# Optimization experiments

Hardware: AMD Instinct MI355X
Metric: run time of the kernel (lower is better)

The kernel has to match this reference:

```python
import jax, jax.numpy as jnp
import numpy as np

B, S, D, H = 4, 2048, 1024, 16
HD = D // H


def setup_inputs() -> dict:
    key = jax.random.key(0)
    ks = jax.random.split(key, 6)
    scale = 1.0 / np.sqrt(D)
    return {
        'x': jax.random.normal(ks[0], (B, S, D), dtype=jnp.float32),
        'wq': jax.random.normal(ks[1], (D, D), dtype=jnp.float32) * scale,
        'wk': jax.random.normal(ks[2], (D, D), dtype=jnp.float32) * scale,
        'wv': jax.random.normal(ks[3], (D, D), dtype=jnp.float32) * scale,
        'wo': jax.random.normal(ks[4], (D, D), dtype=jnp.float32) * scale,
        'wo_b': jnp.zeros((D,), dtype=jnp.float32),
    }


def reference(x, wq, wk, wv, wo, wo_b):
    b, s, _ = x.shape
    # Linear projections (torch Linear: x @ W.T), reshape to [b, h, s, hd]
    def proj(w):
        return jnp.einsum('bsd,ed->bse', x, w).reshape(b, s, H, HD).transpose(0, 2, 1, 3)
    q, k, v = proj(wq), proj(wk), proj(wv)
    scores = jnp.einsum('bhqd,bhkd->bhqk', q, k)  # [b,h,s,s]
    causal = jnp.triu(jnp.ones((s, s), dtype=bool), k=1)
    scores = jnp.where(causal, -jnp.inf, scores)
    attn = jax.nn.softmax(scores / np.sqrt(HD), axis=-1)
    ctx = jnp.einsum('bhqk,bhkd->bhqd', attn, v)  # [b,h,s,hd]
    ctx = ctx.transpose(0, 2, 1, 3).reshape(b, s, D)
    return jnp.einsum('bsd,ed->bse', ctx, wo) + wo_b
```

## Files before the change

kernel.cpp:

```cpp
#include <hip/hip_runtime.h>

#define SB 4
#define SS 2048
#define SD 1024
#define SH 16
#define SHD 64
#define SM (SB * SS)

typedef __bf16 bf16x8 __attribute__((ext_vector_type(8)));
typedef float f32x4 __attribute__((ext_vector_type(4)));

static __device__ __forceinline__ unsigned short f2bf(float x) {
    unsigned int u = __builtin_bit_cast(unsigned int, x);
    u += 0x7fffu + ((u >> 16) & 1u);
    return (unsigned short)(u >> 16);
}

static __device__ __forceinline__ float fast_exp2(float x) {
#if __has_builtin(__builtin_amdgcn_exp2f)
    return __builtin_amdgcn_exp2f(x);
#else
    return exp2f(x);
#endif
}

static __device__ __forceinline__ unsigned int pkhi(float a, float b) {
    return __builtin_amdgcn_perm(__builtin_bit_cast(unsigned int, a),
                                 __builtin_bit_cast(unsigned int, b), 0x07060302u);
}

typedef __attribute__((address_space(1))) void GV;
typedef __attribute__((address_space(3))) void LV;

static __device__ __forceinline__ void async16(const void* g, void* l) {
    __builtin_amdgcn_global_load_lds((GV*)g, (LV*)l, 16, 0, 0);
}

#define QSCALE 0.18033688011112042f

__global__ __launch_bounds__(256) void cast_all(
    const float* __restrict__ x,  const float* __restrict__ wq,
    const float* __restrict__ wk, const float* __restrict__ wv,
    const float* __restrict__ wo,
    unsigned short* __restrict__ xb, unsigned short* __restrict__ wqkv,
    unsigned short* __restrict__ wo16) {
    int i = blockIdx.x * 256 + threadIdx.x;
    const float4* src;
    ushort4* dst;
    if (i < 2097152) {
        src = reinterpret_cast<const float4*>(x) + i;
        dst = reinterpret_cast<ushort4*>(xb) + i;
    } else {
        int j = i - 2097152;
        int which = j >> 18;
        int r = j & 262143;
        const float* ws_[4] = {wq, wk, wv, wo};
        src = reinterpret_cast<const float4*>(ws_[which]) + r;
        dst = (which < 3 ? reinterpret_cast<ushort4*>(wqkv) + which * 262144
                         : reinterpret_cast<ushort4*>(wo16)) + r;
    }
    float4 v = *src;
    ushort4 o;
    o.x = f2bf(v.x); o.y = f2bf(v.y); o.z = f2bf(v.z); o.w = f2bf(v.w);
    *dst = o;
}

#define NT16 (SD / 64)

__device__ __forceinline__ void gemm_mainloop(
    const unsigned short* __restrict__ A,
    const unsigned short* __restrict__ Bt,
    int tileM, int tileN, int tid,
    unsigned short* As0, unsigned short* As1, unsigned short* As2,
    unsigned short* Bs0, unsigned short* Bs1,
    f32x4 (&acc)[4][4]) {

    const int lane = tid & 63;
    const int quad = lane >> 4;
    const int col0 = lane & 15;
    const int w = tid >> 6;
    const int wm = w >> 1;
    const int wn = w & 1;

    const int r0 = tid >> 3;
    const int cc = ((tid & 7) ^ (r0 & 7)) * 8;

    const unsigned short* gA0 = A + (size_t)(tileM + r0) * SD + cc;
    const unsigned short* gA1 = gA0 + (size_t)64 * SD;
    const unsigned short* gA2 = gA0 + (size_t)128 * SD;
    const unsigned short* gA3 = gA0 + (size_t)192 * SD;
    const unsigned short* gB0 = Bt + (size_t)(tileN + r0) * SD + cc;
    const unsigned short* gB1 = gB0 + (size_t)64 * SD;

    unsigned short* const Asb[3] = {As0, As1, As2};
    unsigned short* const Bsb[2] = {Bs0, Bs1};
    const int t16 = tid * 16;

    const int cs0 = (quad ^ (col0 & 7)) * 16;
    const int cs1 = ((4 + quad) ^ (col0 & 7)) * 16;
    const int arow = (wm * 64 + col0) * 128;
    const int brow = (wn * 64 + col0) * 128;

#define STAGE_A(t, Asx) do {                                         \
        async16(gA0 + (t) * 64, (char*)(Asx) + t16);                 \
        async16(gA1 + (t) * 64, (char*)(Asx) + 8192 + t16);          \
        async16(gA2 + (t) * 64, (char*)(Asx) + 16384 + t16);         \
        async16(gA3 + (t) * 64, (char*)(Asx) + 24576 + t16);         \
    } while (0)
#define STAGE_B(t, Bsx) do {                                         \
        async16(gB0 + (t) * 64, (char*)(Bsx) + t16);                 \
        async16(gB1 + (t) * 64, (char*)(Bsx) + 8192 + t16);          \
    } while (0)

    STAGE_A(0, As0);
    STAGE_B(0, Bs0);
    STAGE_A(1, As1);

#pragma unroll
    for (int t = 0; t < NT16; ++t) {
        if (t + 1 < NT16)
            asm volatile("s_waitcnt vmcnt(4)" ::: "memory");
        else
            asm volatile("s_waitcnt vmcnt(0)" ::: "memory");
        __builtin_amdgcn_s_barrier();
        __builtin_amdgcn_sched_barrier(0);

        const unsigned short* As = Asb[t % 3];
        const unsigned short* Bs = Bsb[t & 1];

        bf16x8 af[4][2], bfr[4][2];
#pragma unroll
        for (int fr = 0; fr < 4; ++fr) {
            const char* rp = (const char*)As + arow + fr * 2048;
            af[fr][0] = *reinterpret_cast<const bf16x8*>(rp + cs0);
            af[fr][1] = *reinterpret_cast<const bf16x8*>(rp + cs1);
        }
#pragma unroll
        for (int fc = 0; fc < 4; ++fc) {
            const char* rp = (const char*)Bs + brow + fc * 2048;
            bfr[fc][0] = *reinterpret_cast<const bf16x8*>(rp + cs0);
            bfr[fc][1] = *reinterpret_cast<const bf16x8*>(rp + cs1);
        }

        if (t + 1 < NT16) STAGE_B(t + 1, Bsb[(t + 1) & 1]);
        if (t + 2 < NT16) STAGE_A(t + 2, Asb[(t + 2) % 3]);

        __builtin_amdgcn_s_setprio(1);
#pragma unroll
        for (int ks = 0; ks < 2; ++ks)
#pragma unroll
            for (int fr = 0; fr < 4; ++fr)
#pragma unroll
                for (int fc = 0; fc < 4; ++fc)
                    acc[fr][fc] = __builtin_amdgcn_mfma_f32_16x16x32_bf16(
                        af[fr][ks], bfr[fc][ks], acc[fr][fc], 0, 0, 0);
        __builtin_amdgcn_s_setprio(0);
    }
#undef STAGE_A
#undef STAGE_B
}

__global__ __launch_bounds__(512, 2) void gemm_qkv(
    const unsigned short* __restrict__ xb,
    const unsigned short* __restrict__ wqkv,
    unsigned short* __restrict__ Qd,
    unsigned short* __restrict__ Kd,
    unsigned short* __restrict__ Vtd) {

    __shared__ __align__(16) unsigned short As0[256 * 64];
    __shared__ __align__(16) unsigned short As1[256 * 64];
    __shared__ __align__(16) unsigned short As2[256 * 64];
    __shared__ __align__(16) unsigned short Bs0[128 * 64];
    __shared__ __align__(16) unsigned short Bs1[128 * 64];
    const int tid = threadIdx.x;
    const int tileN = blockIdx.x * 128;
    const int tileM = blockIdx.y * 256;

    f32x4 acc[4][4];
    const f32x4 z = {0.f, 0.f, 0.f, 0.f};
#pragma unroll
    for (int i = 0; i < 4; ++i)
#pragma unroll
        for (int j = 0; j < 4; ++j) acc[i][j] = z;

    gemm_mainloop(xb, wqkv, tileM, tileN, tid, As0, As1, As2, Bs0, Bs1, acc);

    const int lane = tid & 63, quad = lane >> 4, col0 = lane & 15;
    const int w = tid >> 6, wm = w >> 1, wn = w & 1;

#pragma unroll
    for (int ct = 0; ct < 4; ++ct) {
        int n0 = tileN + wn * 64 + ct * 16;
        int which = n0 >> 10;
        int e0 = n0 & 1023;
        int h = e0 >> 6;
        int hd = (e0 & 63) + col0;
#pragma unroll
        for (int rt = 0; rt < 4; ++rt) {
            int m0 = tileM + wm * 64 + rt * 16 + quad * 4;
            int bb = m0 >> 11;
            int s0 = m0 & 2047;
            int bh = bb * SH + h;
            if (which == 0) {
                int base = (bh * SS + s0) * SHD + hd;
#pragma unroll
                for (int r = 0; r < 4; ++r)
                    Qd[base + r * SHD] = f2bf(acc[rt][ct][r] * QSCALE);
            } else if (which == 1) {
                int base = (bh * SS + s0) * SHD + hd;
#pragma unroll
                for (int r = 0; r < 4; ++r)
                    Kd[base + r * SHD] = f2bf(acc[rt][ct][r]);
            } else {
                int base = (bh * SHD + hd) * SS + s0;
                ushort4 pk;
                pk.x = f2bf(acc[rt][ct][0]);
                pk.y = f2bf(acc[rt][ct][1]);
                pk.z = f2bf(acc[rt][ct][2]);
                pk.w = f2bf(acc[rt][ct][3]);
                *reinterpret_cast<ushort4*>(Vtd + base) = pk;
            }
        }
    }
}

__global__ __launch_bounds__(512, 2) void gemm_out(
    const unsigned short* __restrict__ ctx,
    const unsigned short* __restrict__ wo16,
    const float* __restrict__ wb,
    float* __restrict__ out) {

    __shared__ __align__(16) unsigned short As0[256 * 64];
    __shared__ __align__(16) unsigned short As1[256 * 64];
    __shared__ __align__(16) unsigned short As2[256 * 64];
    __shared__ __align__(16) unsigned short Bs0[128 * 64];
    __shared__ __align__(16) unsigned short Bs1[128 * 64];
    const int tid = threadIdx.x;
    const int tileN = blockIdx.x * 128;
    const int tileM = blockIdx.y * 256;

    f32x4 acc[4][4];
    const f32x4 z = {0.f, 0.f, 0.f, 0.f};
#pragma unroll
    for (int i = 0; i < 4; ++i)
#pragma unroll
        for (int j = 0; j < 4; ++j) acc[i][j] = z;

    gemm_mainloop(ctx, wo16, tileM, tileN, tid, As0, As1, As2, Bs0, Bs1, acc);

    const int lane = tid & 63, quad = lane >> 4, col0 = lane & 15;
    const int w = tid >> 6, wm = w >> 1, wn = w & 1;

#pragma unroll
    for (int ct = 0; ct < 4; ++ct) {
        int n = tileN + wn * 64 + ct * 16 + col0;
        float bias = wb[n];
#pragma unroll
        for (int rt = 0; rt < 4; ++rt) {
            int m0 = tileM + wm * 64 + rt * 16 + quad * 4;
#pragma unroll
            for (int r = 0; r < 4; ++r)
                out[(size_t)(m0 + r) * SD + n] = acc[rt][ct][r] + bias;
        }
    }
}

#define PSTR 72

__device__ __forceinline__ void stage_kv(
    const unsigned short* __restrict__ Kg,
    const unsigned short* __restrict__ Vtg,
    size_t base, int t, int srow0, int scs, int tid,
    unsigned short* Kb, unsigned short* Vb) {
#pragma unroll
    for (int j = 0; j < 2; ++j) {
        int row = j * 32 + srow0;
        int chunk = scs ^ (row & 7);
        int slot16 = (j * 256 + tid) * 16;
        async16(Kg + base + (size_t)(t * 64 + row) * SHD + chunk * 8,
                (char*)Kb + slot16);
        async16(Vtg + base + (size_t)row * SS + t * 64 + chunk * 8,
                (char*)Vb + slot16);
    }
}

__device__ __forceinline__ void attn_tile(
    const unsigned short* __restrict__ Kc,
    const unsigned short* __restrict__ Vc,
    int kb, int q0, int quad, int col0,
    const bf16x8 (&bq)[2][2], const bf16x8& ones,
    unsigned short* Psw, f32x4 (&ot)[2][4], f32x4 (&lacc)[2]) {

    const f32x4 z = {0.f, 0.f, 0.f, 0.f};

    bf16x8 ak[4][2];
#pragma unroll
    for (int rt = 0; rt < 4; ++rt)
#pragma unroll
        for (int ks = 0; ks < 2; ++ks)
            ak[rt][ks] = *reinterpret_cast<const bf16x8*>(
                &Kc[(rt * 16 + col0) * 64 + ((ks * 4 + quad) ^ (col0 & 7)) * 8]);

    f32x4 sc[2][4];
#pragma unroll
    for (int g = 0; g < 2; ++g)
#pragma unroll
        for (int rt = 0; rt < 4; ++rt) sc[g][rt] = z;
#pragma unroll
    for (int rt = 0; rt < 4; ++rt)
#pragma unroll
        for (int g = 0; g < 2; ++g) {
            sc[g][rt] = __builtin_amdgcn_mfma_f32_16x16x32_bf16(
                ak[rt][0], bq[g][0], sc[g][rt], 0, 0, 0);
            sc[g][rt] = __builtin_amdgcn_mfma_f32_16x16x32_bf16(
                ak[rt][1], bq[g][1], sc[g][rt], 0, 0, 0);
        }

    if (kb + 63 > q0) {
#pragma unroll
        for (int g = 0; g < 2; ++g) {
            int q = q0 + g * 16 + col0;
#pragma unroll
            for (int rt = 0; rt < 4; ++rt)
#pragma unroll
                for (int r = 0; r < 4; ++r) {
                    int key = kb + rt * 16 + quad * 4 + r;
                    if (key > q) sc[g][rt][r] = -3.0e38f;
                }
        }
    }

#pragma unroll
    for (int g = 0; g < 2; ++g)
#pragma unroll
        for (int rt = 0; rt < 4; ++rt)
#pragma unroll
            for (int r = 0; r < 4; ++r)
                sc[g][rt][r] = fast_exp2(sc[g][rt][r]);

    bf16x8 bp[2][2];
#pragma unroll
    for (int g = 0; g < 2; ++g) {
#pragma unroll
        for (int rt = 0; rt < 4; ++rt) {
            uint2 pk;
            pk.x = pkhi(sc[g][rt][1], sc[g][rt][0]);
            pk.y = pkhi(sc[g][rt][3], sc[g][rt][2]);
            *reinterpret_cast<uint2*>(&Psw[col0 * PSTR + rt * 16 + quad * 4]) = pk;
        }
#pragma unroll
        for (int ks = 0; ks < 2; ++ks)
            bp[g][ks] = *reinterpret_cast<const bf16x8*>(
                &Psw[col0 * PSTR + ks * 32 + quad * 8]);
    }

#pragma unroll
    for (int ks = 0; ks < 2; ++ks) {
        lacc[0] = __builtin_amdgcn_mfma_f32_16x16x32_bf16(ones, bp[0][ks], lacc[0], 0, 0, 0);
        lacc[1] = __builtin_amdgcn_mfma_f32_16x16x32_bf16(ones, bp[1][ks], lacc[1], 0, 0, 0);
#pragma unroll
        for (int ct = 0; ct < 4; ++ct) {
            bf16x8 av = *reinterpret_cast<const bf16x8*>(
                &Vc[(ct * 16 + col0) * 64 + ((ks * 4 + quad) ^ (col0 & 7)) * 8]);
            ot[0][ct] = __builtin_amdgcn_mfma_f32_16x16x32_bf16(av, bp[0][ks], ot[0][ct], 0, 0, 0);
            ot[1][ct] = __builtin_amdgcn_mfma_f32_16x16x32_bf16(av, bp[1][ks], ot[1][ct], 0, 0, 0);
        }
    }
}

__device__ __forceinline__ void attn_pass(
    const unsigned short* __restrict__ Qg,
    const unsigned short* __restrict__ Kg,
    const unsigned short* __restrict__ Vtg,
    unsigned short* __restrict__ ctx,
    size_t base, int b, int h, int jj,
    int tid, int w, int quad, int col0,
    unsigned short* K0, unsigned short* K1, unsigned short* K2, unsigned short* K3,
    unsigned short* V0, unsigned short* V1, unsigned short* V2, unsigned short* V3,
    unsigned short* Psw, const bf16x8& ones) {

    const int q0 = jj * 128 + w * 32;
    const int qlim = q0 + 31;

    bf16x8 bq[2][2];
#pragma unroll
    for (int g = 0; g < 2; ++g)
#pragma unroll
        for (int ks = 0; ks < 2; ++ks)
            bq[g][ks] = *reinterpret_cast<const bf16x8*>(
                Qg + base + (size_t)(q0 + g * 16 + col0) * SHD + ks * 32 + quad * 8);

    f32x4 ot[2][4], lacc[2];
    const f32x4 z = {0.f, 0.f, 0.f, 0.f};
#pragma unroll
    for (int g = 0; g < 2; ++g) {
        lacc[g] = z;
#pragma unroll
        for (int ct = 0; ct < 4; ++ct) ot[g][ct] = z;
    }

    const int srow0 = tid >> 3;
    const int scs = tid & 7;
    const int nkt = 2 * jj + 2;

    __syncthreads();
    stage_kv(Kg, Vtg, base, 0, srow0, scs, tid, K0, V0);
    if (1 < nkt) stage_kv(Kg, Vtg, base, 1, srow0, scs, tid, K1, V1);

#pragma unroll 1
    for (int kt = 0; kt < nkt; kt += 4) {
        __syncthreads();
        if (kt + 2 < nkt) stage_kv(Kg, Vtg, base, kt + 2, srow0, scs, tid, K2, V2);
        if (kt + 3 < nkt) stage_kv(Kg, Vtg, base, kt + 3, srow0, scs, tid, K3, V3);
        if (kt * 64 <= qlim)
            attn_tile(K0, V0, kt * 64, q0, quad, col0, bq, ones, Psw, ot, lacc);
        if ((kt + 1) * 64 <= qlim)
            attn_tile(K1, V1, (kt + 1) * 64, q0, quad, col0, bq, ones, Psw, ot, lacc);

        if (kt + 2 >= nkt) break;
        __syncthreads();
        if (kt + 4 < nkt) stage_kv(Kg, Vtg, base, kt + 4, srow0, scs, tid, K0, V0);
        if (kt + 5 < nkt) stage_kv(Kg, Vtg, base, kt + 5, srow0, scs, tid, K1, V1);
        if ((kt + 2) * 64 <= qlim)
            attn_tile(K2, V2, (kt + 2) * 64, q0, quad, col0, bq, ones, Psw, ot, lacc);
        if (kt + 3 < nkt && (kt + 3) * 64 <= qlim)
            attn_tile(K3, V3, (kt + 3) * 64, q0, quad, col0, bq, ones, Psw, ot, lacc);
    }

#pragma unroll
    for (int g = 0; g < 2; ++g) {
        float inv = 1.0f / lacc[g][0];
        int q = q0 + g * 16 + col0;
        size_t obase = ((size_t)b * SS + q) * SD + h * SHD;
#pragma unroll
        for (int ct = 0; ct < 4; ++ct) {
            uint2 pk;
            pk.x = pkhi(ot[g][ct][1] * inv, ot[g][ct][0] * inv);
            pk.y = pkhi(ot[g][ct][3] * inv, ot[g][ct][2] * inv);
            *reinterpret_cast<uint2*>(ctx + obase + ct * 16 + quad * 4) = pk;
        }
    }
}

__global__ __launch_bounds__(256) void attn_kernel(
    const unsigned short* __restrict__ Qg,
    const unsigned short* __restrict__ Kg,
    const unsigned short* __restrict__ Vtg,
    unsigned short* __restrict__ ctx) {

    __shared__ __align__(16) unsigned short K0[64 * 64];
    __shared__ __align__(16) unsigned short K1[64 * 64];
    __shared__ __align__(16) unsigned short K2[64 * 64];
    __shared__ __align__(16) unsigned short K3[64 * 64];
    __shared__ __align__(16) unsigned short V0[64 * 64];
    __shared__ __align__(16) unsigned short V1[64 * 64];
    __shared__ __align__(16) unsigned short V2[64 * 64];
    __shared__ __align__(16) unsigned short V3[64 * 64];
    __shared__ __align__(16) unsigned short Ps[4 * 16 * PSTR];

    const int tid = threadIdx.x;
    const int w = tid >> 6;
    const int lane = tid & 63;
    const int quad = lane >> 4;
    const int col0 = lane & 15;
    const int bh = blockIdx.y;
    const int b = bh >> 4;
    const int h = bh & 15;
    const size_t base = (size_t)bh * (SS * SHD);
    unsigned short* Psw = Ps + w * 16 * PSTR;

    bf16x8 ones;
#pragma unroll
    for (int i = 0; i < 8; ++i) ones[i] = (__bf16)1.0f;

    attn_pass(Qg, Kg, Vtg, ctx, base, b, h, blockIdx.x,
              tid, w, quad, col0, K0, K1, K2, K3, V0, V1, V2, V3, Psw, ones);
    attn_pass(Qg, Kg, Vtg, ctx, base, b, h, 15 - blockIdx.x,
              tid, w, quad, col0, K0, K1, K2, K3, V0, V1, V2, V3, Psw, ones);
}

extern "C" void kernel_launch(void* const* d_in, const int* in_sizes, int n_in,
                              void* d_out, int out_size, void* d_ws, size_t ws_size,
                              hipStream_t stream) {
    const float* x  = (const float*)d_in[0];
    const float* wq = (const float*)d_in[1];
    const float* wk = (const float*)d_in[2];
    const float* wv = (const float*)d_in[3];
    const float* wo = (const float*)d_in[4];
    const float* wb = (const float*)d_in[5];
    float* out = (float*)d_out;

    char* ws = (char*)d_ws;
    unsigned short* xb   = (unsigned short*)(ws + 0);
    unsigned short* wqkv = (unsigned short*)(ws + 16777216);
    unsigned short* q    = (unsigned short*)(ws + 23068672);
    unsigned short* k    = (unsigned short*)(ws + 39845888);
    unsigned short* vt   = (unsigned short*)(ws + 56623104);
    unsigned short* ctx  = (unsigned short*)(ws + 73400320);
    unsigned short* wo16 = (unsigned short*)(ws + 90177536);

    cast_all<<<12288, 256, 0, stream>>>(x, wq, wk, wv, wo, xb, wqkv, wo16);

    gemm_qkv<<<dim3(3 * SD / 128, SM / 256), 512, 0, stream>>>(xb, wqkv, q, k, vt);

    attn_kernel<<<dim3(8, SB * SH), 256, 0, stream>>>(q, k, vt, ctx);

    gemm_out<<<dim3(SD / 128, SM / 256), 512, 0, stream>>>(ctx, wo16, wb, out);
}
```

Baseline: 242.5 us.

## Rewrite QKV GEMM with 256x256 tiles and ping-pong phased pipeline

Replaces the QKV projection GEMM with a 256x256 block tile, where each of eight waves computes a 128x64 sub-tile. The main loop is unrolled into two LDS buffer sets (even/odd k-steps) and split into barrier-synchronised phases. Each phase interleaves LDS fragment reads, async global-to-LDS copies for later k-steps, and a quarter of the MFMA work. The aim is more operand reuse per loaded byte and better overlap of memory traffic with matrix math. The cost is more accumulator registers (128 floats per thread), 128KB of LDS per block, and half as many blocks in the grid (384).

```diff
diff --git a/kernel.cpp b/kernel.cpp
--- a/kernel.cpp
+++ b/kernel.cpp
@@ -65,6 +65,206 @@
     *dst = o;
 }
 
+#define NIT 8
+
+#define PH_SYNC do { __builtin_amdgcn_s_barrier();                        \
+        asm volatile("s_waitcnt lgkmcnt(0)" ::: "memory");                \
+        __builtin_amdgcn_sched_barrier(0); } while (0)
+
+__global__ __launch_bounds__(512, 2) void gemm_qkv(
+    const unsigned short* __restrict__ xb,
+    const unsigned short* __restrict__ wqkv,
+    unsigned short* __restrict__ Qd,
+    unsigned short* __restrict__ Kd,
+    unsigned short* __restrict__ Vtd) {
+
+    __shared__ __align__(16) unsigned short Ae[256 * 64];
+    __shared__ __align__(16) unsigned short Be[256 * 64];
+    __shared__ __align__(16) unsigned short Ao[256 * 64];
+    __shared__ __align__(16) unsigned short Bo[256 * 64];
+
+    const int tid = threadIdx.x;
+    const int tileN = blockIdx.x * 256;
+    const int tileM = blockIdx.y * 256;
+    const int lane = tid & 63;
+    const int quad = lane >> 4;
+    const int col0 = lane & 15;
+    const int w = tid >> 6;
+    const int wm = w >> 2;
+    const int wn = w & 3;
+
+    const int r0 = tid >> 3;
+    const int cc = ((tid & 7) ^ (r0 & 7)) * 8;
+    const unsigned short* pA = xb   + (size_t)(tileM + r0) * SD + cc;
+    const unsigned short* pB = wqkv + (size_t)(tileN + r0) * SD + cc;
+    const int t16 = tid * 16;
+
+#define SQA(t, h, buf) do {                                                    \
+        async16(pA + (size_t)((h) * 128     ) * SD + (t) * 64,                 \
+                (char*)(buf) + (h) * 16384 + t16);                             \
+        async16(pA + (size_t)((h) * 128 + 64) * SD + (t) * 64,                 \
+                (char*)(buf) + (h) * 16384 + 8192 + t16);                      \
+    } while (0)
+#define SQB(t, h, buf) do {                                                    \
+        async16(pB + (size_t)((h) * 128     ) * SD + (t) * 64,                 \
+                (char*)(buf) + (h) * 16384 + t16);                             \
+        async16(pB + (size_t)((h) * 128 + 64) * SD + (t) * 64,                 \
+                (char*)(buf) + (h) * 16384 + 8192 + t16);                      \
+    } while (0)
+
+    const int cs0 = (quad ^ (col0 & 7)) * 16;
+    const int cs1 = ((4 + quad) ^ (col0 & 7)) * 16;
+    const int arowA = (wm * 128 + col0) * 128;
+    const int browB = (wn * 64 + col0) * 128;
+
+    bf16x8 af[4][2], bf[4][2];
+    f32x4 acc[8][4];
+    const f32x4 z = {0.f, 0.f, 0.f, 0.f};
+#pragma unroll
+    for (int i = 0; i < 8; ++i)
+#pragma unroll
+        for (int j = 0; j < 4; ++j) acc[i][j] = z;
+
+#define RDA(buf, fmh) do {                                                     \
+        _Pragma("unroll")                                                      \
+        for (int i_ = 0; i_ < 4; ++i_) {                                       \
+            const char* rp_ = (const char*)(buf) + arowA + ((fmh) + i_) * 2048;\
+            af[i_][0] = *reinterpret_cast<const bf16x8*>(rp_ + cs0);           \
+            af[i_][1] = *reinterpret_cast<const bf16x8*>(rp_ + cs1);           \
+        } } while (0)
+#define RDB(buf, fnh) do {                                                     \
+        _Pragma("unroll")                                                      \
+        for (int n_ = 0; n_ < 2; ++n_) {                                       \
+            const char* rp_ = (const char*)(buf) + browB + ((fnh)*2 + n_) * 2048;\
+            bf[(fnh)*2 + n_][0] = *reinterpret_cast<const bf16x8*>(rp_ + cs0); \
+            bf[(fnh)*2 + n_][1] = *reinterpret_cast<const bf16x8*>(rp_ + cs1); \
+        } } while (0)
+
+#define MFQ(fmb, fnb) do {                                                     \
+        __builtin_amdgcn_s_setprio(1);                                         \
+        _Pragma("unroll")                                                      \
+        for (int ks_ = 0; ks_ < 2; ++ks_)                                      \
+            _Pragma("unroll")                                                  \
+            for (int i_ = 0; i_ < 4; ++i_)                                     \
+                _Pragma("unroll")                                              \
+                for (int n_ = 0; n_ < 2; ++n_)                                 \
+                    acc[(fmb)+i_][(fnb)+n_] =                                  \
+                        __builtin_amdgcn_mfma_f32_16x16x32_bf16(               \
+                            af[i_][ks_], bf[(fnb)+n_][ks_],                    \
+                            acc[(fmb)+i_][(fnb)+n_], 0, 0, 0);                 \
+        __builtin_amdgcn_s_setprio(0);                                         \
+    } while (0)
+
+    SQA(0, 0, Ae); SQA(0, 1, Ae); SQB(0, 0, Be); SQB(0, 1, Be);
+    SQB(1, 0, Bo); SQA(1, 0, Ao);
+    asm volatile("s_waitcnt vmcnt(4)" ::: "memory");
+    __builtin_amdgcn_s_barrier();
+
+#pragma unroll 1
+    for (int j = 0; j < NIT - 1; ++j) {
+        const int t1 = 2 * j + 1, t2 = 2 * j + 2, t3 = 2 * j + 3;
+        RDA(Ae, 0); RDB(Be, 0);
+        SQA(t1, 1, Ao);
+        PH_SYNC; MFQ(0, 0);
+        __builtin_amdgcn_s_barrier();
+        RDB(Be, 1);
+        SQB(t1, 1, Bo);
+        PH_SYNC; MFQ(0, 2);
+        __builtin_amdgcn_s_barrier();
+        RDA(Ae, 4);
+        SQB(t2, 0, Be);
+        PH_SYNC; MFQ(4, 0);
+        __builtin_amdgcn_s_barrier();
+        SQA(t2, 0, Ae);
+        PH_SYNC; MFQ(4, 2);
+        asm volatile("s_waitcnt vmcnt(4)" ::: "memory");
+        __builtin_amdgcn_s_barrier();
+        RDA(Ao, 0); RDB(Bo, 0);
+        SQA(t2, 1, Ae);
+        PH_SYNC; MFQ(0, 0);
+        __builtin_amdgcn_s_barrier();
+        RDB(Bo, 1);
+        SQB(t2, 1, Be);
+        PH_SYNC; MFQ(0, 2);
+        __builtin_amdgcn_s_barrier();
+        RDA(Ao, 4);
+        SQB(t3, 0, Bo);
+        PH_SYNC; MFQ(4, 0);
+        __builtin_amdgcn_s_barrier();
+        SQA(t3, 0, Ao);
+        PH_SYNC; MFQ(4, 2);
+        asm volatile("s_waitcnt vmcnt(4)" ::: "memory");
+        __builtin_amdgcn_s_barrier();
+    }
+
+    {
+        RDA(Ae, 0); RDB(Be, 0);
+        SQA(15, 1, Ao);
+        PH_SYNC; MFQ(0, 0);
+        __builtin_amdgcn_s_barrier();
+        RDB(Be, 1);
+        SQB(15, 1, Bo);
+        PH_SYNC; MFQ(0, 2);
+        __builtin_amdgcn_s_barrier();
+        RDA(Ae, 4);
+        PH_SYNC; MFQ(4, 0);
+        __builtin_amdgcn_s_barrier();
+        PH_SYNC; MFQ(4, 2);
+        asm volatile("s_waitcnt vmcnt(0)" ::: "memory");
+        __builtin_amdgcn_s_barrier();
+        RDA(Ao, 0); RDB(Bo, 0);
+        PH_SYNC; MFQ(0, 0);
+        __builtin_amdgcn_s_barrier();
+        RDB(Bo, 1);
+        PH_SYNC; MFQ(0, 2);
+        __builtin_amdgcn_s_barrier();
+        RDA(Ao, 4);
+        PH_SYNC; MFQ(4, 0);
+        __builtin_amdgcn_s_barrier();
+        PH_SYNC; MFQ(4, 2);
+    }
+#undef SQA
+#undef SQB
+#undef RDA
+#undef RDB
+#undef MFQ
+
+#pragma unroll
+    for (int fn = 0; fn < 4; ++fn) {
+        int n0 = tileN + wn * 64 + fn * 16;
+        int which = n0 >> 10;
+        int e0 = n0 & 1023;
+        int h = e0 >> 6;
+        int hd = (e0 & 63) + col0;
+#pragma unroll
+        for (int fm = 0; fm < 8; ++fm) {
+            int m0 = tileM + wm * 128 + fm * 16 + quad * 4;
+            int bb = m0 >> 11;
+            int s0 = m0 & 2047;
+            int bh = bb * SH + h;
+            if (which == 0) {
+                int base = (bh * SS + s0) * SHD + hd;
+#pragma unroll
+                for (int r = 0; r < 4; ++r)
+                    Qd[base + r * SHD] = f2bf(acc[fm][fn][r] * QSCALE);
+            } else if (which == 1) {
+                int base = (bh * SS + s0) * SHD + hd;
+#pragma unroll
+                for (int r = 0; r < 4; ++r)
+                    Kd[base + r * SHD] = f2bf(acc[fm][fn][r]);
+            } else {
+                int base = (bh * SHD + hd) * SS + s0;
+                ushort4 pk;
+                pk.x = f2bf(acc[fm][fn][0]);
+                pk.y = f2bf(acc[fm][fn][1]);
+                pk.z = f2bf(acc[fm][fn][2]);
+                pk.w = f2bf(acc[fm][fn][3]);
+                *reinterpret_cast<ushort4*>(Vtd + base) = pk;
+            }
+        }
+    }
+}
+
 #define NT16 (SD / 64)
 
 __device__ __forceinline__ void gemm_mainloop(
@@ -160,70 +360,6 @@
 #undef STAGE_B
 }
 
-__global__ __launch_bounds__(512, 2) void gemm_qkv(
-    const unsigned short* __restrict__ xb,
-    const unsigned short* __restrict__ wqkv,
-    unsigned short* __restrict__ Qd,
-    unsigned short* __restrict__ Kd,
-    unsigned short* __restrict__ Vtd) {
-
-    __shared__ __align__(16) unsigned short As0[256 * 64];
-    __shared__ __align__(16) unsigned short As1[256 * 64];
-    __shared__ __align__(16) unsigned short As2[256 * 64];
-    __shared__ __align__(16) unsigned short Bs0[128 * 64];
-    __shared__ __align__(16) unsigned short Bs1[128 * 64];
-    const int tid = threadIdx.x;
-    const int tileN = blockIdx.x * 128;
-    const int tileM = blockIdx.y * 256;
-
-    f32x4 acc[4][4];
-    const f32x4 z = {0.f, 0.f, 0.f, 0.f};
-#pragma unroll
-    for (int i = 0; i < 4; ++i)
-#pragma unroll
-        for (int j = 0; j < 4; ++j) acc[i][j] = z;
-
-    gemm_mainloop(xb, wqkv, tileM, tileN, tid, As0, As1, As2, Bs0, Bs1, acc);
-
-    const int lane = tid & 63, quad = lane >> 4, col0 = lane & 15;
-    const int w = tid >> 6, wm = w >> 1, wn = w & 1;
-
-#pragma unroll
-    for (int ct = 0; ct < 4; ++ct) {
-        int n0 = tileN + wn * 64 + ct * 16;
-        int which = n0 >> 10;
-        int e0 = n0 & 1023;
-        int h = e0 >> 6;
-        int hd = (e0 & 63) + col0;
-#pragma unroll
-        for (int rt = 0; rt < 4; ++rt) {
-            int m0 = tileM + wm * 64 + rt * 16 + quad * 4;
-            int bb = m0 >> 11;
-            int s0 = m0 & 2047;
-            int bh = bb * SH + h;
-            if (which == 0) {
-                int base = (bh * SS + s0) * SHD + hd;
-#pragma unroll
-                for (int r = 0; r < 4; ++r)
-                    Qd[base + r * SHD] = f2bf(acc[rt][ct][r] * QSCALE);
-            } else if (which == 1) {
-                int base = (bh * SS + s0) * SHD + hd;
-#pragma unroll
-                for (int r = 0; r < 4; ++r)
-                    Kd[base + r * SHD] = f2bf(acc[rt][ct][r]);
-            } else {
-                int base = (bh * SHD + hd) * SS + s0;
-                ushort4 pk;
-                pk.x = f2bf(acc[rt][ct][0]);
-                pk.y = f2bf(acc[rt][ct][1]);
-                pk.z = f2bf(acc[rt][ct][2]);
-                pk.w = f2bf(acc[rt][ct][3]);
-                *reinterpret_cast<ushort4*>(Vtd + base) = pk;
-            }
-        }
-    }
-}
-
 __global__ __launch_bounds__(512, 2) void gemm_out(
     const unsigned short* __restrict__ ctx,
     const unsigned short* __restrict__ wo16,
@@ -501,7 +637,7 @@
 
     cast_all<<<12288, 256, 0, stream>>>(x, wq, wk, wv, wo, xb, wqkv, wo16);
 
-    gemm_qkv<<<dim3(3 * SD / 128, SM / 256), 512, 0, stream>>>(xb, wqkv, q, k, vt);
+    gemm_qkv<<<dim3(3 * SD / 256, SM / 256), 512, 0, stream>>>(xb, wqkv, q, k, vt);
 
     attn_kernel<<<dim3(8, SB * SH), 256, 0, stream>>>(q, k, vt, ctx);
 
```

Measured after the change: 253.8 us. +4.7%, slower.
